# Kernel optimization log

Measured on AMD Instinct MI355X. Metric: run time of the kernel, lower is better.

## Reference

```python
import jax, jax.numpy as jnp
import numpy as np

B, N1, N2 = 16, 4096, 1024
C1, C2 = 128, 256
IN_CH, OUT_CH = 4096, 256  # fc1 acts on N1 dim due to transpose; BN channels = C2 = OUT_CH
BN_EPS = 1e-5


def setup_inputs() -> dict:
    key = jax.random.key(0)
    ks = jax.random.split(key, 8)
    x1 = jax.random.normal(ks[0], (B, N1, C1), dtype=jnp.float32)
    x2 = jax.random.normal(ks[1], (B, N2, C2), dtype=jnp.float32)
    xyz1 = jax.random.normal(ks[2], (B, N1, 3), dtype=jnp.float32)
    xyz2 = jax.random.normal(ks[3], (B, N2, 3), dtype=jnp.float32)
    # Linear(in_channels=N1 -> out_channels) params, PyTorch default init scale
    bound = 1.0 / np.sqrt(IN_CH)
    W1 = jax.random.uniform(ks[4], (OUT_CH, IN_CH), jnp.float32, -bound, bound)
    b1 = jax.random.uniform(ks[5], (OUT_CH,), jnp.float32, -bound, bound)
    gamma = jnp.ones((OUT_CH,), jnp.float32)
    beta = jnp.zeros((OUT_CH,), jnp.float32)
    return {"x1": x1, "x2": x2, "xyz1": xyz1, "xyz2": xyz2,
            "W1": W1, "b1": b1, "gamma": gamma, "beta": beta}


def _square_distance(src, dst):
    # src: [B,N,3], dst: [B,M,3] -> [B,N,M]
    d = -2.0 * jnp.einsum('bnc,bmc->bnm', src, dst)
    d = d + jnp.sum(src * src, -1)[:, :, None]
    d = d + jnp.sum(dst * dst, -1)[:, None, :]
    return d


def reference(x1, x2, xyz1, xyz2, W1, b1, gamma, beta):
    dists = _square_distance(xyz1, xyz2)              # [B,N1,N2]
    neg3, idx = jax.lax.top_k(-dists, 3)              # 3 smallest distances
    d3 = -neg3                                        # [B,N1,3], ascending
    dist_recip = 1.0 / (d3 + 1e-8)
    weight = dist_recip / jnp.sum(dist_recip, axis=2, keepdims=True)
    gathered = jax.vmap(lambda pts, i: pts[i])(x2, idx)   # [B,N1,3,C2]
    interp = jnp.sum(gathered * weight[..., None], axis=2)  # [B,N1,C2]
    t = jnp.swapaxes(interp, 1, 2)                    # [B,C2,N1]
    y = jnp.einsum('bcn,on->bco', t, W1) + b1         # [B,C2,OUT_CH]
    # BatchNorm1d over channel dim 1 (size C2 == OUT_CH), training-mode batch stats
    mean = jnp.mean(y, axis=(0, 2), keepdims=True)
    var = jnp.mean((y - mean) ** 2, axis=(0, 2), keepdims=True)
    y = (y - mean) / jnp.sqrt(var + BN_EPS)
    y = gamma[None, :, None] * y + beta[None, :, None]
    y = jax.nn.relu(y)
    return jnp.swapaxes(y, 1, 2)                      # [B,OUT_CH,C2]
```

## Files before the change

### kernel.cpp

```cpp
#include <hip/hip_runtime.h>
#include <hip/hip_bf16.h>
#include <float.h>

#define B_    16
#define N1_   4096
#define N2_   1024
#define C2_   256
#define OUT_  256
#define K_    4096
#define SPLITK 8
#define KCH_  (K_ / SPLITK)
#define ZSLAB 1048576

typedef short short8 __attribute__((ext_vector_type(8)));
typedef float float4v __attribute__((ext_vector_type(4)));

static __device__ __forceinline__ unsigned short f32_to_bf16_bits(float v) {
    __hip_bfloat16 h = __float2bfloat16(v);
    return *(unsigned short*)&h;
}

__global__ __launch_bounds__(256) void w1cvt_kernel(
    const float* __restrict__ W1, unsigned short* __restrict__ W1b)
{
    const int i = (blockIdx.x * 256 + threadIdx.x) * 4;
    float4 v = *(const float4*)(W1 + i);
    ushort4 o;
    o.x = f32_to_bf16_bits(v.x);
    o.y = f32_to_bf16_bits(v.y);
    o.z = f32_to_bf16_bits(v.z);
    o.w = f32_to_bf16_bits(v.w);
    *(ushort4*)(W1b + i) = o;
}

#define TPAD 65
struct KnnSh {
    float4 pts[N2_];
    float  pf[4][64][3];
};
union ShUnion {
    KnnSh a;
    unsigned short tile[C2_][TPAD];
};

__global__ __launch_bounds__(256) void knn_interp_kernel(
    const float* __restrict__ xyz1,
    const float* __restrict__ xyz2,
    const float* __restrict__ x2,
    unsigned short* __restrict__ interp_t)
{
    __shared__ ShUnion sh;
    __shared__ float rw[64][3];
    __shared__ int   ri[64][3];

    const int b  = blockIdx.y;
    const int n0 = blockIdx.x * 64;
    const int t  = threadIdx.x;
    const int w  = t >> 6;
    const int l  = t & 63;

    for (int r = 0; r < 4; ++r) {
        int j = r * 256 + t;
        const float* p = xyz2 + ((size_t)b * N2_ + j) * 3;
        float x = p[0], y = p[1], z = p[2];
        sh.a.pts[j] = make_float4(x, y, z, 0.5f * ((x * x + y * y) + z * z));
    }
    __syncthreads();

    const int n1 = n0 + l;
    const float* q = xyz1 + ((size_t)b * N1_ + n1) * 3;
    const float s0 = q[0], s1 = q[1], s2 = q[2];
    const float ns0 = -s0, ns1 = -s1, ns2 = -s2;
    const float ss = (s0 * s0 + s1 * s1) + s2 * s2;

    const int jbase = w << 8;
    float f0 = FLT_MAX, f1 = FLT_MAX, f2 = FLT_MAX;

    #pragma unroll 4
    for (int jj = 0; jj < 256; ++jj) {
        const int j = jbase + jj;
        float4 pq = sh.a.pts[j];
        float acc = fmaf(ns0, pq.x, pq.w);
        acc = fmaf(ns1, pq.y, acc);
        acc = fmaf(ns2, pq.z, acc);
        float dk = fmaxf(fmaf(2.0f, acc, ss), 0.0f);
        float fp = __int_as_float((__float_as_int(dk) & 0xFFFFFC00) | j);
        float nf0 = fminf(fp, f0);
        float nf1 = __builtin_amdgcn_fmed3f(fp, f0, f1);
        float nf2 = fminf(f2, fmaxf(fp, f1));
        f0 = nf0; f1 = nf1; f2 = nf2;
    }

    sh.a.pf[w][l][0] = f0; sh.a.pf[w][l][1] = f1; sh.a.pf[w][l][2] = f2;
    __syncthreads();

    if (w == 0) {
        float g0 = FLT_MAX, g1 = FLT_MAX, g2 = FLT_MAX;
        #pragma unroll
        for (int p = 0; p < 4; ++p)
        #pragma unroll
        for (int r = 0; r < 3; ++r) {
            float fp = sh.a.pf[p][l][r];
            float n0v = fminf(fp, g0);
            float n1v = __builtin_amdgcn_fmed3f(fp, g0, g1);
            float n2v = fminf(g2, fmaxf(fp, g1));
            g0 = n0v; g1 = n1v; g2 = n2v;
        }
        int j0 = __float_as_int(g0) & 1023;
        int j1 = __float_as_int(g1) & 1023;
        int j2 = __float_as_int(g2) & 1023;
        const float4 p0 = sh.a.pts[j0];
        const float4 p1 = sh.a.pts[j1];
        const float4 p2 = sh.a.pts[j2];
        float d0 = ss + 2.0f * (p0.w - ((s0 * p0.x + s1 * p0.y) + s2 * p0.z));
        float d1 = ss + 2.0f * (p1.w - ((s0 * p1.x + s1 * p1.y) + s2 * p1.z));
        float d2 = ss + 2.0f * (p2.w - ((s0 * p2.x + s1 * p2.y) + s2 * p2.z));
        float r0 = 1.0f / (d0 + 1e-8f);
        float r1 = 1.0f / (d1 + 1e-8f);
        float r2 = 1.0f / (d2 + 1e-8f);
        float s  = (r0 + r1) + r2;
        rw[l][0] = r0 / s;  rw[l][1] = r1 / s;  rw[l][2] = r2 / s;
        ri[l][0] = j0;      ri[l][1] = j1;      ri[l][2] = j2;
    }
    __syncthreads();

    for (int p = 0; p < 16; ++p) {
        int nl = p * 4 + w;
        float w0 = rw[nl][0], w1 = rw[nl][1], w2 = rw[nl][2];
        int i0g = ri[nl][0], i1g = ri[nl][1], i2g = ri[nl][2];
        const float4 va = ((const float4*)(x2 + ((size_t)b * N2_ + i0g) * C2_))[l];
        const float4 vb = ((const float4*)(x2 + ((size_t)b * N2_ + i1g) * C2_))[l];
        const float4 vc = ((const float4*)(x2 + ((size_t)b * N2_ + i2g) * C2_))[l];
        float fa[4] = {va.x, va.y, va.z, va.w};
        float fb[4] = {vb.x, vb.y, vb.z, vb.w};
        float fc[4] = {vc.x, vc.y, vc.z, vc.w};
        #pragma unroll
        for (int i = 0; i < 4; ++i) {
            float v = w0 * fa[i];
            v = fmaf(w1, fb[i], v);
            v = fmaf(w2, fc[i], v);
            sh.tile[l * 4 + i][nl] = f32_to_bf16_bits(v);
        }
    }
    __syncthreads();

    for (int r = 0; r < 64; ++r) {
        int c = r * 4 + w;
        interp_t[((size_t)b * C2_ + c) * K_ + n0 + l] = sh.tile[c][l];
    }
}

#define LDA 40
__global__ __launch_bounds__(256) void gemm_kernel(
    const unsigned short* __restrict__ W1b,
    const unsigned short* __restrict__ interp_t,
    float* __restrict__ Zp)
{
    __shared__ unsigned short Alds[64][LDA];
    __shared__ unsigned short Blds[64][LDA];
    const int z  = blockIdx.z;
    const int b  = z >> 3;
    const int kc = z & 7;
    const int o0 = blockIdx.y * 64;
    const int c0 = blockIdx.x * 64;
    const int t = threadIdx.x;
    const int w = t >> 6, l = t & 63;
    const int row = t >> 2, q = t & 3;
    const int ob = (w >> 1) * 32, cb = (w & 1) * 32;
    const int m = l & 15, kq = l >> 4;

    const unsigned short* Wp = W1b + (size_t)(o0 + row) * K_ + kc * KCH_ + q * 8;
    const unsigned short* Bp = interp_t + ((size_t)b * C2_ + (c0 + row)) * K_ + kc * KCH_ + q * 8;

    float4v acc[2][2] = {};

    for (int kk = 0; kk < KCH_; kk += 32) {
        uint4 av = *(const uint4*)(Wp + kk);
        uint4 bv = *(const uint4*)(Bp + kk);
        *(uint4*)&Alds[row][q * 8] = av;
        *(uint4*)&Blds[row][q * 8] = bv;
        __syncthreads();
        short8 a0 = *(const short8*)&Alds[ob + m][kq * 8];
        short8 a1 = *(const short8*)&Alds[ob + 16 + m][kq * 8];
        short8 b0 = *(const short8*)&Blds[cb + m][kq * 8];
        short8 b1f = *(const short8*)&Blds[cb + 16 + m][kq * 8];
        acc[0][0] = __builtin_amdgcn_mfma_f32_16x16x32_bf16(a0, b0,  acc[0][0], 0, 0, 0);
        acc[0][1] = __builtin_amdgcn_mfma_f32_16x16x32_bf16(a0, b1f, acc[0][1], 0, 0, 0);
        acc[1][0] = __builtin_amdgcn_mfma_f32_16x16x32_bf16(a1, b0,  acc[1][0], 0, 0, 0);
        acc[1][1] = __builtin_amdgcn_mfma_f32_16x16x32_bf16(a1, b1f, acc[1][1], 0, 0, 0);
        __syncthreads();
    }

    float* Zslab = Zp + (size_t)kc * ZSLAB;
    #pragma unroll
    for (int mi = 0; mi < 2; ++mi)
    #pragma unroll
    for (int ni = 0; ni < 2; ++ni)
    #pragma unroll
    for (int r = 0; r < 4; ++r) {
        int o = o0 + ob + mi * 16 + kq * 4 + r;
        int c = c0 + cb + ni * 16 + m;
        Zslab[((size_t)b * OUT_ + o) * C2_ + c] = acc[mi][ni][r];
    }
}

__global__ __launch_bounds__(256) void reduce_stats_kernel(
    float* __restrict__ Zp, const float* __restrict__ b1,
    float* __restrict__ accum)
{
    const int b  = blockIdx.x >> 4;
    const int oq = blockIdx.x & 15;
    const int c  = threadIdx.x;
    float s = 0.0f, s2 = 0.0f;
    for (int o16 = 0; o16 < 16; ++o16) {
        int o = oq * 16 + o16;
        size_t base = ((size_t)b * OUT_ + o) * C2_ + c;
        float v = b1[o];
        #pragma unroll
        for (int sl = 0; sl < SPLITK; ++sl)
            v += Zp[base + (size_t)sl * ZSLAB];
        Zp[base] = v;
        s += v; s2 += v * v;
    }
    atomicAdd(&accum[c], s);
    atomicAdd(&accum[C2_ + c], s2);
}

__global__ __launch_bounds__(256) void bn_kernel(
    const float* __restrict__ Z, const float* __restrict__ accum,
    const float* __restrict__ gamma, const float* __restrict__ beta,
    float* __restrict__ out)
{
    const int i = (blockIdx.x * 256 + threadIdx.x) * 4;
    float4 z = *(const float4*)(Z + i);
    float vals[4] = {z.x, z.y, z.z, z.w};
    const int cb = i & 255;
    float res[4];
    #pragma unroll
    for (int j = 0; j < 4; ++j) {
        int c = cb + j;
        float mean = accum[c] * (1.0f / 4096.0f);
        float var  = accum[C2_ + c] * (1.0f / 4096.0f) - mean * mean;
        float rstd = 1.0f / sqrtf(var + 1e-5f);
        float v = gamma[c] * ((vals[j] - mean) * rstd) + beta[c];
        res[j] = fmaxf(v, 0.0f);
    }
    *(float4*)(out + i) = make_float4(res[0], res[1], res[2], res[3]);
}

extern "C" void kernel_launch(void* const* d_in, const int* in_sizes, int n_in,
                              void* d_out, int out_size, void* d_ws, size_t ws_size,
                              hipStream_t stream) {
    const float* x2    = (const float*)d_in[1];
    const float* xyz1  = (const float*)d_in[2];
    const float* xyz2  = (const float*)d_in[3];
    const float* W1    = (const float*)d_in[4];
    const float* b1    = (const float*)d_in[5];
    const float* gamma = (const float*)d_in[6];
    const float* beta  = (const float*)d_in[7];

    char* ws = (char*)d_ws;
    unsigned short* interp_t = (unsigned short*)(ws);
    unsigned short* W1b      = (unsigned short*)(ws + 33554432);
    float*          Zp       = (float*)(ws + 35651584);
    float*          accum    = (float*)(ws + 69206016);

    (void)hipMemsetAsync(accum, 0, 512 * sizeof(float), stream);

    w1cvt_kernel      <<<1024, 256, 0, stream>>>(W1, W1b);
    knn_interp_kernel <<<dim3(64, 16), 256, 0, stream>>>(xyz1, xyz2, x2, interp_t);
    gemm_kernel       <<<dim3(4, 4, 128), 256, 0, stream>>>(W1b, interp_t, Zp);
    reduce_stats_kernel<<<256, 256, 0, stream>>>(Zp, b1, accum);
    bn_kernel         <<<1024, 256, 0, stream>>>(Zp, accum, gamma, beta,
                                                 (float*)d_out);
}
```

Before: 164.4 us.

## Process two query points per thread in KNN kernel and fold accum memset

After: 179.3 us. 9.1% more time.

```diff
diff --git a/kernel.cpp b/kernel.cpp
--- a/kernel.cpp
+++ b/kernel.cpp
@@ -21,8 +21,13 @@
 }
 
 __global__ __launch_bounds__(256) void w1cvt_kernel(
-    const float* __restrict__ W1, unsigned short* __restrict__ W1b)
-{
+    const float* __restrict__ W1, unsigned short* __restrict__ W1b,
+    float* __restrict__ accum)
+{
+    if (blockIdx.x == 0) {
+        accum[threadIdx.x] = 0.0f;
+        accum[256 + threadIdx.x] = 0.0f;
+    }
     const int i = (blockIdx.x * 256 + threadIdx.x) * 4;
     float4 v = *(const float4*)(W1 + i);
     ushort4 o;
@@ -36,7 +41,7 @@
 #define TPAD 65
 struct KnnSh {
     float4 pts[N2_];
-    float  pf[4][64][3];
+    float  pf[4][128][3];
 };
 union ShUnion {
     KnnSh a;
@@ -50,11 +55,11 @@
     unsigned short* __restrict__ interp_t)
 {
     __shared__ ShUnion sh;
-    __shared__ float rw[64][3];
-    __shared__ int   ri[64][3];
+    __shared__ float rw[128][3];
+    __shared__ int   ri[128][3];
 
     const int b  = blockIdx.y;
-    const int n0 = blockIdx.x * 64;
+    const int n0 = blockIdx.x * 128;
     const int t  = threadIdx.x;
     const int w  = t >> 6;
     const int l  = t & 63;
@@ -67,40 +72,55 @@
     }
     __syncthreads();
 
-    const int n1 = n0 + l;
-    const float* q = xyz1 + ((size_t)b * N1_ + n1) * 3;
-    const float s0 = q[0], s1 = q[1], s2 = q[2];
-    const float ns0 = -s0, ns1 = -s1, ns2 = -s2;
-    const float ss = (s0 * s0 + s1 * s1) + s2 * s2;
+    const float* qa = xyz1 + ((size_t)b * N1_ + n0 + l) * 3;
+    const float* qb = xyz1 + ((size_t)b * N1_ + n0 + 64 + l) * 3;
+    const float sa0 = qa[0], sa1 = qa[1], sa2 = qa[2];
+    const float sb0 = qb[0], sb1 = qb[1], sb2 = qb[2];
+    const float nsa0 = -sa0, nsa1 = -sa1, nsa2 = -sa2;
+    const float nsb0 = -sb0, nsb1 = -sb1, nsb2 = -sb2;
+    const float ssa = (sa0 * sa0 + sa1 * sa1) + sa2 * sa2;
+    const float ssb = (sb0 * sb0 + sb1 * sb1) + sb2 * sb2;
 
     const int jbase = w << 8;
-    float f0 = FLT_MAX, f1 = FLT_MAX, f2 = FLT_MAX;
+    float fa0 = FLT_MAX, fa1 = FLT_MAX, fa2 = FLT_MAX;
+    float fb0 = FLT_MAX, fb1 = FLT_MAX, fb2 = FLT_MAX;
 
     #pragma unroll 4
     for (int jj = 0; jj < 256; ++jj) {
         const int j = jbase + jj;
         float4 pq = sh.a.pts[j];
-        float acc = fmaf(ns0, pq.x, pq.w);
-        acc = fmaf(ns1, pq.y, acc);
-        acc = fmaf(ns2, pq.z, acc);
-        float dk = fmaxf(fmaf(2.0f, acc, ss), 0.0f);
-        float fp = __int_as_float((__float_as_int(dk) & 0xFFFFFC00) | j);
-        float nf0 = fminf(fp, f0);
-        float nf1 = __builtin_amdgcn_fmed3f(fp, f0, f1);
-        float nf2 = fminf(f2, fmaxf(fp, f1));
-        f0 = nf0; f1 = nf1; f2 = nf2;
-    }
-
-    sh.a.pf[w][l][0] = f0; sh.a.pf[w][l][1] = f1; sh.a.pf[w][l][2] = f2;
+        float acca = fmaf(nsa0, pq.x, pq.w);
+        acca = fmaf(nsa1, pq.y, acca);
+        acca = fmaf(nsa2, pq.z, acca);
+        float dka = fmaxf(fmaf(2.0f, acca, ssa), 0.0f);
+        float fpa = __int_as_float((__float_as_int(dka) & 0xFFFFFC00) | j);
+        float na0 = fminf(fpa, fa0);
+        float na1 = __builtin_amdgcn_fmed3f(fpa, fa0, fa1);
+        float na2 = fminf(fa2, fmaxf(fpa, fa1));
+        fa0 = na0; fa1 = na1; fa2 = na2;
+        float accb = fmaf(nsb0, pq.x, pq.w);
+        accb = fmaf(nsb1, pq.y, accb);
+        accb = fmaf(nsb2, pq.z, accb);
+        float dkb = fmaxf(fmaf(2.0f, accb, ssb), 0.0f);
+        float fpb = __int_as_float((__float_as_int(dkb) & 0xFFFFFC00) | j);
+        float nb0 = fminf(fpb, fb0);
+        float nb1 = __builtin_amdgcn_fmed3f(fpb, fb0, fb1);
+        float nb2 = fminf(fb2, fmaxf(fpb, fb1));
+        fb0 = nb0; fb1 = nb1; fb2 = nb2;
+    }
+
+    sh.a.pf[w][l][0] = fa0;      sh.a.pf[w][l][1] = fa1;      sh.a.pf[w][l][2] = fa2;
+    sh.a.pf[w][64 + l][0] = fb0; sh.a.pf[w][64 + l][1] = fb1; sh.a.pf[w][64 + l][2] = fb2;
     __syncthreads();
 
-    if (w == 0) {
+    if (w < 2) {
+        const int ql = w * 64 + l;
         float g0 = FLT_MAX, g1 = FLT_MAX, g2 = FLT_MAX;
         #pragma unroll
         for (int p = 0; p < 4; ++p)
         #pragma unroll
         for (int r = 0; r < 3; ++r) {
-            float fp = sh.a.pf[p][l][r];
+            float fp = sh.a.pf[p][ql][r];
             float n0v = fminf(fp, g0);
             float n1v = __builtin_amdgcn_fmed3f(fp, g0, g1);
             float n2v = fminf(g2, fmaxf(fp, g1));
@@ -109,6 +129,10 @@
         int j0 = __float_as_int(g0) & 1023;
         int j1 = __float_as_int(g1) & 1023;
         int j2 = __float_as_int(g2) & 1023;
+        const float s0 = w ? sb0 : sa0;
+        const float s1 = w ? sb1 : sa1;
+        const float s2 = w ? sb2 : sa2;
+        const float ss = w ? ssb : ssa;
         const float4 p0 = sh.a.pts[j0];
         const float4 p1 = sh.a.pts[j1];
         const float4 p2 = sh.a.pts[j2];
@@ -119,34 +143,37 @@
         float r1 = 1.0f / (d1 + 1e-8f);
         float r2 = 1.0f / (d2 + 1e-8f);
         float s  = (r0 + r1) + r2;
-        rw[l][0] = r0 / s;  rw[l][1] = r1 / s;  rw[l][2] = r2 / s;
-        ri[l][0] = j0;      ri[l][1] = j1;      ri[l][2] = j2;
+        rw[ql][0] = r0 / s;  rw[ql][1] = r1 / s;  rw[ql][2] = r2 / s;
+        ri[ql][0] = j0;      ri[ql][1] = j1;      ri[ql][2] = j2;
     }
     __syncthreads();
 
-    for (int p = 0; p < 16; ++p) {
-        int nl = p * 4 + w;
-        float w0 = rw[nl][0], w1 = rw[nl][1], w2 = rw[nl][2];
-        int i0g = ri[nl][0], i1g = ri[nl][1], i2g = ri[nl][2];
-        const float4 va = ((const float4*)(x2 + ((size_t)b * N2_ + i0g) * C2_))[l];
-        const float4 vb = ((const float4*)(x2 + ((size_t)b * N2_ + i1g) * C2_))[l];
-        const float4 vc = ((const float4*)(x2 + ((size_t)b * N2_ + i2g) * C2_))[l];
-        float fa[4] = {va.x, va.y, va.z, va.w};
-        float fb[4] = {vb.x, vb.y, vb.z, vb.w};
-        float fc[4] = {vc.x, vc.y, vc.z, vc.w};
-        #pragma unroll
-        for (int i = 0; i < 4; ++i) {
-            float v = w0 * fa[i];
-            v = fmaf(w1, fb[i], v);
-            v = fmaf(w2, fc[i], v);
-            sh.tile[l * 4 + i][nl] = f32_to_bf16_bits(v);
+    for (int h = 0; h < 2; ++h) {
+        for (int p = 0; p < 16; ++p) {
+            int nl = h * 64 + p * 4 + w;
+            int col = p * 4 + w;
+            float w0 = rw[nl][0], w1 = rw[nl][1], w2 = rw[nl][2];
+            int i0g = ri[nl][0], i1g = ri[nl][1], i2g = ri[nl][2];
+            const float4 va = ((const float4*)(x2 + ((size_t)b * N2_ + i0g) * C2_))[l];
+            const float4 vb = ((const float4*)(x2 + ((size_t)b * N2_ + i1g) * C2_))[l];
+            const float4 vc = ((const float4*)(x2 + ((size_t)b * N2_ + i2g) * C2_))[l];
+            float fa[4] = {va.x, va.y, va.z, va.w};
+            float fb[4] = {vb.x, vb.y, vb.z, vb.w};
+            float fc[4] = {vc.x, vc.y, vc.z, vc.w};
+            #pragma unroll
+            for (int i = 0; i < 4; ++i) {
+                float v = w0 * fa[i];
+                v = fmaf(w1, fb[i], v);
+                v = fmaf(w2, fc[i], v);
+                sh.tile[l * 4 + i][col] = f32_to_bf16_bits(v);
+            }
         }
-    }
-    __syncthreads();
-
-    for (int r = 0; r < 64; ++r) {
-        int c = r * 4 + w;
-        interp_t[((size_t)b * C2_ + c) * K_ + n0 + l] = sh.tile[c][l];
+        __syncthreads();
+        for (int r = 0; r < 64; ++r) {
+            int c = r * 4 + w;
+            interp_t[((size_t)b * C2_ + c) * K_ + n0 + h * 64 + l] = sh.tile[c][l];
+        }
+        __syncthreads();
     }
 }
 
@@ -265,10 +292,8 @@
     float*          Zp       = (float*)(ws + 35651584);
     float*          accum    = (float*)(ws + 69206016);
 
-    (void)hipMemsetAsync(accum, 0, 512 * sizeof(float), stream);
-
-    w1cvt_kernel      <<<1024, 256, 0, stream>>>(W1, W1b);
-    knn_interp_kernel <<<dim3(64, 16), 256, 0, stream>>>(xyz1, xyz2, x2, interp_t);
+    w1cvt_kernel      <<<1024, 256, 0, stream>>>(W1, W1b, accum);
+    knn_interp_kernel <<<dim3(32, 16), 256, 0, stream>>>(xyz1, xyz2, x2, interp_t);
     gemm_kernel       <<<dim3(4, 4, 128), 256, 0, stream>>>(W1b, interp_t, Zp);
     reduce_stats_kernel<<<256, 256, 0, stream>>>(Zp, b1, accum);
     bn_kernel         <<<1024, 256, 0, stream>>>(Zp, accum, gamma, beta,
```

## Enlarge GEMM tile to 128x64 and fold accum zeroing into W1 conversion

Applied to the files above, without the earlier changes.

Result: no change. 163.0 us (-0.9%).

```diff
diff --git a/kernel.cpp b/kernel.cpp
--- a/kernel.cpp
+++ b/kernel.cpp
@@ -21,8 +21,13 @@
 }
 
 __global__ __launch_bounds__(256) void w1cvt_kernel(
-    const float* __restrict__ W1, unsigned short* __restrict__ W1b)
-{
+    const float* __restrict__ W1, unsigned short* __restrict__ W1b,
+    float* __restrict__ accum)
+{
+    if (blockIdx.x == 0) {
+        accum[threadIdx.x] = 0.0f;
+        accum[256 + threadIdx.x] = 0.0f;
+    }
     const int i = (blockIdx.x * 256 + threadIdx.x) * 4;
     float4 v = *(const float4*)(W1 + i);
     ushort4 o;
@@ -156,44 +161,47 @@
     const unsigned short* __restrict__ interp_t,
     float* __restrict__ Zp)
 {
-    __shared__ unsigned short Alds[64][LDA];
+    __shared__ unsigned short Alds[128][LDA];
     __shared__ unsigned short Blds[64][LDA];
     const int z  = blockIdx.z;
     const int b  = z >> 3;
     const int kc = z & 7;
-    const int o0 = blockIdx.y * 64;
+    const int o0 = blockIdx.y * 128;
     const int c0 = blockIdx.x * 64;
     const int t = threadIdx.x;
     const int w = t >> 6, l = t & 63;
-    const int row = t >> 2, q = t & 3;
-    const int ob = (w >> 1) * 32, cb = (w & 1) * 32;
+    const int arow = t >> 1, ahalf = t & 1;
+    const int brow = t >> 2, bq = t & 3;
+    const int ob = (w >> 1) * 64, cb = (w & 1) * 32;
     const int m = l & 15, kq = l >> 4;
 
-    const unsigned short* Wp = W1b + (size_t)(o0 + row) * K_ + kc * KCH_ + q * 8;
-    const unsigned short* Bp = interp_t + ((size_t)b * C2_ + (c0 + row)) * K_ + kc * KCH_ + q * 8;
-
-    float4v acc[2][2] = {};
+    const unsigned short* Wp = W1b + (size_t)(o0 + arow) * K_ + kc * KCH_ + ahalf * 16;
+    const unsigned short* Bp = interp_t + ((size_t)b * C2_ + (c0 + brow)) * K_ + kc * KCH_ + bq * 8;
+
+    float4v acc[4][2] = {};
 
     for (int kk = 0; kk < KCH_; kk += 32) {
-        uint4 av = *(const uint4*)(Wp + kk);
-        uint4 bv = *(const uint4*)(Bp + kk);
-        *(uint4*)&Alds[row][q * 8] = av;
-        *(uint4*)&Blds[row][q * 8] = bv;
+        uint4 av0 = *(const uint4*)(Wp + kk);
+        uint4 av1 = *(const uint4*)(Wp + kk + 8);
+        uint4 bv  = *(const uint4*)(Bp + kk);
+        *(uint4*)&Alds[arow][ahalf * 16]     = av0;
+        *(uint4*)&Alds[arow][ahalf * 16 + 8] = av1;
+        *(uint4*)&Blds[brow][bq * 8]         = bv;
         __syncthreads();
-        short8 a0 = *(const short8*)&Alds[ob + m][kq * 8];
-        short8 a1 = *(const short8*)&Alds[ob + 16 + m][kq * 8];
-        short8 b0 = *(const short8*)&Blds[cb + m][kq * 8];
-        short8 b1f = *(const short8*)&Blds[cb + 16 + m][kq * 8];
-        acc[0][0] = __builtin_amdgcn_mfma_f32_16x16x32_bf16(a0, b0,  acc[0][0], 0, 0, 0);
-        acc[0][1] = __builtin_amdgcn_mfma_f32_16x16x32_bf16(a0, b1f, acc[0][1], 0, 0, 0);
-        acc[1][0] = __builtin_amdgcn_mfma_f32_16x16x32_bf16(a1, b0,  acc[1][0], 0, 0, 0);
-        acc[1][1] = __builtin_amdgcn_mfma_f32_16x16x32_bf16(a1, b1f, acc[1][1], 0, 0, 0);
+        short8 bf0 = *(const short8*)&Blds[cb + m][kq * 8];
+        short8 bf1 = *(const short8*)&Blds[cb + 16 + m][kq * 8];
+        #pragma unroll
+        for (int mi = 0; mi < 4; ++mi) {
+            short8 af = *(const short8*)&Alds[ob + mi * 16 + m][kq * 8];
+            acc[mi][0] = __builtin_amdgcn_mfma_f32_16x16x32_bf16(af, bf0, acc[mi][0], 0, 0, 0);
+            acc[mi][1] = __builtin_amdgcn_mfma_f32_16x16x32_bf16(af, bf1, acc[mi][1], 0, 0, 0);
+        }
         __syncthreads();
     }
 
     float* Zslab = Zp + (size_t)kc * ZSLAB;
     #pragma unroll
-    for (int mi = 0; mi < 2; ++mi)
+    for (int mi = 0; mi < 4; ++mi)
     #pragma unroll
     for (int ni = 0; ni < 2; ++ni)
     #pragma unroll
@@ -265,11 +273,9 @@
     float*          Zp       = (float*)(ws + 35651584);
     float*          accum    = (float*)(ws + 69206016);
 
-    (void)hipMemsetAsync(accum, 0, 512 * sizeof(float), stream);
-
-    w1cvt_kernel      <<<1024, 256, 0, stream>>>(W1, W1b);
+    w1cvt_kernel      <<<1024, 256, 0, stream>>>(W1, W1b, accum);
     knn_interp_kernel <<<dim3(64, 16), 256, 0, stream>>>(xyz1, xyz2, x2, interp_t);
-    gemm_kernel       <<<dim3(4, 4, 128), 256, 0, stream>>>(W1b, interp_t, Zp);
+    gemm_kernel       <<<dim3(4, 2, 128), 256, 0, stream>>>(W1b, interp_t, Zp);
     reduce_stats_kernel<<<256, 256, 0, stream>>>(Zp, b1, accum);
     bn_kernel         <<<1024, 256, 0, stream>>>(Zp, accum, gamma, beta,
                                                  (float*)d_out);
```
